# Performance work log

Hardware: AMD Instinct MI355X
Metric: run time of the kernel (lower is better)

## Reference

```python
import jax, jax.numpy as jnp
import numpy as np

N_NODES = 50000


def _add_self_loops(edge_index, num_nodes):
    loop = jnp.arange(num_nodes, dtype=edge_index.dtype)
    row = jnp.concatenate([edge_index[0], loop])
    col = jnp.concatenate([edge_index[1], loop])
    return row, col


def _gcn_norm(row, col, num_nodes):
    # deg computed on target index with unit edge weights (PyG gcn_norm)
    deg = jax.ops.segment_sum(jnp.ones_like(col, dtype=jnp.float32), col,
                              num_segments=num_nodes)
    dis = jnp.where(deg > 0, jax.lax.rsqrt(jnp.maximum(deg, 1.0)), 0.0)
    return dis[row] * dis[col]  # [E]


def _gcn_conv(x, W, b, row, col, norm, num_nodes):
    h = x @ W                                  # dense transform first (PyG order)
    msg = h[row] * norm[:, None]               # gather + normalize
    out = jax.ops.segment_sum(msg, col, num_segments=num_nodes)  # scatter-add
    return out + b


def setup_inputs() -> dict:
    key = jax.random.key(0)
    ks = jax.random.split(key, 10)
    E = 800000
    x = jax.random.normal(ks[0], (N_NODES, 29), dtype=jnp.float32)
    edge_index = jax.random.randint(ks[1], (2, E), 0, N_NODES, dtype=jnp.int64)

    def glorot(k, fan_in, fan_out):
        s = jnp.sqrt(2.0 / (fan_in + fan_out)).astype(jnp.float32)
        return jax.random.normal(k, (fan_in, fan_out), dtype=jnp.float32) * s

    return {
        "x": x, "edge_index": edge_index,
        "W1": glorot(ks[2], 29, 96),  "b1": jnp.zeros((96,), jnp.float32),
        "W2": glorot(ks[3], 96, 128), "b2": jnp.zeros((128,), jnp.float32),
        "W3": glorot(ks[4], 128, 64), "b3": jnp.zeros((64,), jnp.float32),
        "W4": glorot(ks[5], 64, 32),  "b4": jnp.zeros((32,), jnp.float32),
    }


def reference(x, edge_index, W1, b1, W2, b2, W3, b3, W4, b4):
    row, col = _add_self_loops(edge_index, N_NODES)
    norm = _gcn_norm(row, col, N_NODES)  # same graph -> same norm for all layers
    h = _gcn_conv(x, W1, b1, row, col, norm, N_NODES)
    h = jax.nn.relu(h)
    # dropout(p=0.4) is identity in eval mode
    h = _gcn_conv(h, W2, b2, row, col, norm, N_NODES)
    h = _gcn_conv(h, W3, b3, row, col, norm, N_NODES)
    h = _gcn_conv(h, W4, b4, row, col, norm, N_NODES)
    return h
```

## Files before the change

### kernel.cpp

```cpp
#include <hip/hip_runtime.h>


constexpr int NN  = 50000;
constexpr int CAP = 64;
constexpr int AGB = (NN * 8 + 255) / 256;
constexpr int C1B = (NN + 255) / 256;
constexpr int PREPB = (NN * 32 + 64 + 255) / 256;
constexpr int W34XB = 17;
constexpr int W234XB = 13;
constexpr int PGB = 128;
constexpr int SLICE = (800000 + PGB - 1) / PGB;

typedef unsigned short u16;

__global__ void place_x_kernel(const int* __restrict__ row, const int* __restrict__ col,
                               int* __restrict__ cnt, u16* __restrict__ ell, int E) {
    const int g  = blockIdx.x & 7;
    const int bi = blockIdx.x >> 3;
    const int e0 = bi * SLICE;
    int e1 = e0 + SLICE; if (e1 > E) e1 = E;
    for (int e = e0 + threadIdx.x; e < e1; e += 256) {
        const int c = col[e];
        if ((unsigned)c >= (unsigned)NN || ((c >> 6) & 7) != g) continue;
        const int r = row[e];
        if ((unsigned)r >= (unsigned)NN) continue;
        const int pos = atomicAdd(&cnt[c], 1);
        if (pos < CAP) ell[c * CAP + pos] = (u16)r;
    }
}

__global__ void prep_all_kernel(const int* __restrict__ cnt, u16* __restrict__ ell,
                                const float* __restrict__ x, float* __restrict__ dis,
                                float* __restrict__ Ba, float* __restrict__ Bb,
                                float* __restrict__ c1d,
                                const float* __restrict__ W3, const float* __restrict__ W4,
                                const float* __restrict__ b3,
                                float* __restrict__ W34, float* __restrict__ v1) {
    if (blockIdx.x >= PREPB) {
        const int wid = (blockIdx.x - PREPB) * 256 + threadIdx.x;
        if (wid < 4096) {
            const int r = wid >> 5, j = wid & 31;
            float a = 0.f;
#pragma unroll 8
            for (int k = 0; k < 64; ++k) a = fmaf(W3[r * 64 + k], W4[k * 32 + j], a);
            W34[wid] = a;
        } else if (wid < 4128) {
            const int j = wid - 4096;
            float a = 0.f;
#pragma unroll 8
            for (int k = 0; k < 64; ++k) a = fmaf(b3[k], W4[k * 32 + j], a);
            v1[j] = a;
        }
        return;
    }
    const int idx = blockIdx.x * blockDim.x + threadIdx.x;
    if (idx < NN * 32) {
        const int n = idx >> 5, f = idx & 31;
        int m = cnt[n]; if (m > CAP) m = CAP;
        const float d = rsqrtf((float)m + 1.0f);
        Ba[idx] = (f < 29) ? x[n * 29 + f] * d : 0.f;
        if (f == 31) dis[n] = d;
        if (f == 30) {
            int mp = (m + 7) & ~7; if (mp > CAP) mp = CAP;
            for (int k = m; k < mp; ++k) ell[n * CAP + k] = (u16)NN;
        }
    } else {
        const int i = idx - NN * 32;
        if (i < 32) { Ba[NN * 32 + i] = 0.f; Bb[NN * 32 + i] = 0.f; }
        else if (i == 32) dis[NN] = 0.f;
        else if (i == 33) c1d[NN] = 0.f;
    }
}

template<int MODE>
__device__ __forceinline__ void agg32_body(const float* __restrict__ hs,
                                           const int* __restrict__ cnt,
                                           const u16* __restrict__ ell,
                                           const float* __restrict__ dis,
                                           const float* __restrict__ c1,
                                           const float* __restrict__ c2,
                                           const float* __restrict__ v1,
                                           const float* __restrict__ v2,
                                           const float* __restrict__ bv,
                                           float* __restrict__ out) {
    const int idx = blockIdx.x * blockDim.x + threadIdx.x;
    if (idx >= NN * 8) return;
    const int n = idx >> 3, c = idx & 7;
    const float4* hpc = (const float4*)hs + c;
    float4 acc = hpc[n * 8];
    int m = cnt[n]; if (m > CAP) m = CAP;
    const int m8 = (m + 7) >> 3;
    const int4* ip = (const int4*)(ell + (size_t)n * CAP);
    int t = 0;
    for (; t + 2 <= m8; t += 2) {
        const int4 sA = ip[t], sB = ip[t + 1];
        const unsigned ax = (unsigned)sA.x, ay = (unsigned)sA.y;
        const unsigned az = (unsigned)sA.z, aw = (unsigned)sA.w;
        const unsigned bx = (unsigned)sB.x, by = (unsigned)sB.y;
        const unsigned bz = (unsigned)sB.z, bw = (unsigned)sB.w;
        const float4 g0 = hpc[(ax & 0xFFFFu) * 8], g1 = hpc[(ax >> 16) * 8];
        const float4 g2 = hpc[(ay & 0xFFFFu) * 8], g3 = hpc[(ay >> 16) * 8];
        const float4 g4 = hpc[(az & 0xFFFFu) * 8], g5 = hpc[(az >> 16) * 8];
        const float4 g6 = hpc[(aw & 0xFFFFu) * 8], g7 = hpc[(aw >> 16) * 8];
        const float4 h0 = hpc[(bx & 0xFFFFu) * 8], h1 = hpc[(bx >> 16) * 8];
        const float4 h2 = hpc[(by & 0xFFFFu) * 8], h3 = hpc[(by >> 16) * 8];
        const float4 h4 = hpc[(bz & 0xFFFFu) * 8], h5 = hpc[(bz >> 16) * 8];
        const float4 h6 = hpc[(bw & 0xFFFFu) * 8], h7 = hpc[(bw >> 16) * 8];
        acc.x += (((g0.x + g1.x) + (g2.x + g3.x)) + ((g4.x + g5.x) + (g6.x + g7.x)))
               + (((h0.x + h1.x) + (h2.x + h3.x)) + ((h4.x + h5.x) + (h6.x + h7.x)));
        acc.y += (((g0.y + g1.y) + (g2.y + g3.y)) + ((g4.y + g5.y) + (g6.y + g7.y)))
               + (((h0.y + h1.y) + (h2.y + h3.y)) + ((h4.y + h5.y) + (h6.y + h7.y)));
        acc.z += (((g0.z + g1.z) + (g2.z + g3.z)) + ((g4.z + g5.z) + (g6.z + g7.z)))
               + (((h0.z + h1.z) + (h2.z + h3.z)) + ((h4.z + h5.z) + (h6.z + h7.z)));
        acc.w += (((g0.w + g1.w) + (g2.w + g3.w)) + ((g4.w + g5.w) + (g6.w + g7.w)))
               + (((h0.w + h1.w) + (h2.w + h3.w)) + ((h4.w + h5.w) + (h6.w + h7.w)));
    }
    if (t < m8) {
        const int4 s = ip[t];
        const unsigned ux = (unsigned)s.x, uy = (unsigned)s.y;
        const unsigned uz = (unsigned)s.z, uw = (unsigned)s.w;
        const float4 g0 = hpc[(ux & 0xFFFFu) * 8], g1 = hpc[(ux >> 16) * 8];
        const float4 g2 = hpc[(uy & 0xFFFFu) * 8], g3 = hpc[(uy >> 16) * 8];
        const float4 g4 = hpc[(uz & 0xFFFFu) * 8], g5 = hpc[(uz >> 16) * 8];
        const float4 g6 = hpc[(uw & 0xFFFFu) * 8], g7 = hpc[(uw >> 16) * 8];
        acc.x += ((g0.x + g1.x) + (g2.x + g3.x)) + ((g4.x + g5.x) + (g6.x + g7.x));
        acc.y += ((g0.y + g1.y) + (g2.y + g3.y)) + ((g4.y + g5.y) + (g6.y + g7.y));
        acc.z += ((g0.z + g1.z) + (g2.z + g3.z)) + ((g4.z + g5.z) + (g6.z + g7.z));
        acc.w += ((g0.w + g1.w) + (g2.w + g3.w)) + ((g4.w + g5.w) + (g6.w + g7.w));
    }
    const float d = dis[n];
    float4 r;
    if (MODE == 0) {
        r.x = acc.x * d; r.y = acc.y * d; r.z = acc.z * d; r.w = acc.w * d;
    } else if (MODE == 1) {
        const float d2 = d * d;
        r.x = acc.x * d2; r.y = acc.y * d2; r.z = acc.z * d2; r.w = acc.w * d2;
    } else {
        const float a1 = c1[n], a2 = c2[n];
        const float4 w1 = ((const float4*)v1)[c];
        const float4 w2 = ((const float4*)v2)[c];
        const float4 bb = ((const float4*)bv)[c];
        r.x = fmaf(acc.x, d, fmaf(a1, w1.x, fmaf(a2, w2.x, bb.x)));
        r.y = fmaf(acc.y, d, fmaf(a1, w1.y, fmaf(a2, w2.y, bb.y)));
        r.z = fmaf(acc.z, d, fmaf(a1, w1.z, fmaf(a2, w2.z, bb.z)));
        r.w = fmaf(acc.w, d, fmaf(a1, w1.w, fmaf(a2, w2.w, bb.w)));
    }
    ((float4*)out)[idx] = r;
}

__device__ __forceinline__ void agg1_body(const float* __restrict__ in,
                                          const int* __restrict__ cnt,
                                          const u16* __restrict__ ell,
                                          const float* __restrict__ dis,
                                          float* __restrict__ out,
                                          float* __restrict__ outd, int blk0) {
    const int n = (blockIdx.x - blk0) * 256 + threadIdx.x;
    if (n >= NN) return;
    float acc = in[n];
    int m = cnt[n]; if (m > CAP) m = CAP;
    const int m8 = (m + 7) >> 3;
    const int4* ip = (const int4*)(ell + (size_t)n * CAP);
    for (int t = 0; t < m8; ++t) {
        const int4 s = ip[t];
        const unsigned ux = (unsigned)s.x, uy = (unsigned)s.y;
        const unsigned uz = (unsigned)s.z, uw = (unsigned)s.w;
        acc += ((in[ux & 0xFFFFu] + in[ux >> 16]) + (in[uy & 0xFFFFu] + in[uy >> 16]))
             + ((in[uz & 0xFFFFu] + in[uz >> 16]) + (in[uw & 0xFFFFu] + in[uw >> 16]));
    }
    const float r = dis[n] * acc;
    out[n] = r;
    if (outd) outd[n] = r * dis[n];
}

__global__ void agg_pre_kernel(const float* __restrict__ Ba, const int* __restrict__ cnt,
                               const u16* __restrict__ ell, const float* __restrict__ dis,
                               float* __restrict__ Bb, float* __restrict__ c1,
                               float* __restrict__ c1d,
                               const float* __restrict__ W2, const float* __restrict__ b2,
                               const float* __restrict__ W34, float* __restrict__ W234,
                               float* __restrict__ v2) {
    if (blockIdx.x < AGB) {
        agg32_body<0>(Ba, cnt, ell, dis, nullptr, nullptr, nullptr, nullptr, nullptr, Bb);
    } else if (blockIdx.x < AGB + C1B) {
        agg1_body(dis, cnt, ell, dis, c1, c1d, AGB);
    } else {
        const int wid = (blockIdx.x - AGB - C1B) * 256 + threadIdx.x;
        if (wid < 3072) {
            const int r = wid >> 5, j = wid & 31;
            float a = 0.f;
#pragma unroll 8
            for (int k = 0; k < 128; ++k) a = fmaf(W2[r * 128 + k], W34[k * 32 + j], a);
            W234[wid] = a;
        } else if (wid < 3104) {
            const int j = wid - 3072;
            float a = 0.f;
#pragma unroll 8
            for (int k = 0; k < 128; ++k) a = fmaf(b2[k], W34[k * 32 + j], a);
            v2[j] = a;
        }
    }
}

__global__ void agg_hop1_kernel(const float* __restrict__ Ba, const int* __restrict__ cnt,
                                const u16* __restrict__ ell, const float* __restrict__ dis,
                                float* __restrict__ Bb, const float* __restrict__ c1d,
                                float* __restrict__ c2) {
    if (blockIdx.x < AGB)
        agg32_body<1>(Ba, cnt, ell, dis, nullptr, nullptr, nullptr, nullptr, nullptr, Bb);
    else
        agg1_body(c1d, cnt, ell, dis, c2, nullptr, AGB);
}

__global__ void agg_hop2_kernel(const float* __restrict__ Bb, const int* __restrict__ cnt,
                                const u16* __restrict__ ell, const float* __restrict__ dis,
                                float* __restrict__ Ba) {
    agg32_body<1>(Bb, cnt, ell, dis, nullptr, nullptr, nullptr, nullptr, nullptr, Ba);
}

__global__ void agg_hop3_kernel(const float* __restrict__ Ba, const int* __restrict__ cnt,
                                const u16* __restrict__ ell, const float* __restrict__ dis,
                                const float* __restrict__ c1, const float* __restrict__ c2,
                                const float* __restrict__ v1, const float* __restrict__ v2,
                                const float* __restrict__ bv, float* __restrict__ out) {
    agg32_body<2>(Ba, cnt, ell, dis, c1, c2, v1, v2, bv, out);
}

__global__ void __launch_bounds__(192, 2)
gemm_fused_kernel(const float* __restrict__ X, const float* __restrict__ W1,
                  const float* __restrict__ b1, const float* __restrict__ dis,
                  const float* __restrict__ W234, float* __restrict__ G) {
    constexpr int NPB = 16, RSX = 36, RSH = 104;
    __shared__ float xs[NPB * RSX];
    __shared__ float hsm[NPB * RSH];
    const int tid = threadIdx.x;
    const int n0  = blockIdx.x * NPB;

    const float4* Xv = (const float4*)(X + (size_t)n0 * 32);
    for (int i = tid; i < NPB * 8; i += 192) {
        const int nl = i >> 3, r = i & 7;
        float4 v = make_float4(0.f, 0.f, 0.f, 0.f);
        if (n0 + nl < NN) v = Xv[nl * 8 + r];
        *(float4*)(xs + nl * RSX + r * 4) = v;
    }
    __syncthreads();

    {
        const int cg = tid % 24, g = tid / 24;
        const float* x0 = xs + (2 * g) * RSX;
        const float* x1 = x0 + RSX;
        const float4* Wv = (const float4*)W1;
        float4 a0 = make_float4(0.f, 0.f, 0.f, 0.f);
        float4 a1 = make_float4(0.f, 0.f, 0.f, 0.f);
#pragma unroll
        for (int k = 0; k < 29; ++k) {
            const float4 w = Wv[k * 24 + cg];
            const float v0 = x0[k], v1 = x1[k];
            a0.x = fmaf(v0, w.x, a0.x); a0.y = fmaf(v0, w.y, a0.y);
            a0.z = fmaf(v0, w.z, a0.z); a0.w = fmaf(v0, w.w, a0.w);
            a1.x = fmaf(v1, w.x, a1.x); a1.y = fmaf(v1, w.y, a1.y);
            a1.z = fmaf(v1, w.z, a1.z); a1.w = fmaf(v1, w.w, a1.w);
        }
        const float4 bb = ((const float4*)b1)[cg];
#pragma unroll
        for (int h = 0; h < 2; ++h) {
            const int nl = 2 * g + h, node = n0 + nl;
            const float d = (node < NN) ? dis[node] : 0.f;
            const float4 a = h ? a1 : a0;
            float4 r;
            r.x = fmaxf(a.x + bb.x, 0.f) * d; r.y = fmaxf(a.y + bb.y, 0.f) * d;
            r.z = fmaxf(a.z + bb.z, 0.f) * d; r.w = fmaxf(a.w + bb.w, 0.f) * d;
            *(float4*)(hsm + nl * RSH + cg * 4) = r;
        }
    }
    __syncthreads();

    if (tid < 128) {
        const int nl = tid >> 3, cg = tid & 7;
        const float* hr = hsm + nl * RSH;
        const float4* Wv = (const float4*)W234;
        float4 a = make_float4(0.f, 0.f, 0.f, 0.f);
#pragma unroll 8
        for (int k = 0; k < 96; ++k) {
            const float4 w = Wv[k * 8 + cg];
            const float v = hr[k];
            a.x = fmaf(v, w.x, a.x); a.y = fmaf(v, w.y, a.y);
            a.z = fmaf(v, w.z, a.z); a.w = fmaf(v, w.w, a.w);
        }
        const int node = n0 + nl;
        if (node < NN) ((float4*)(G + (size_t)node * 32))[cg] = a;
    }
}

extern "C" void kernel_launch(void* const* d_in, const int* in_sizes, int n_in,
                              void* d_out, int out_size, void* d_ws, size_t ws_size,
                              hipStream_t stream) {
    const float* x  = (const float*)d_in[0];
    const int*   ei = (const int*)d_in[1];
    const float* W1 = (const float*)d_in[2]; const float* b1 = (const float*)d_in[3];
    const float* W2 = (const float*)d_in[4]; const float* b2 = (const float*)d_in[5];
    const float* W3 = (const float*)d_in[6]; const float* b3 = (const float*)d_in[7];
    const float* W4 = (const float*)d_in[8]; const float* b4p = (const float*)d_in[9];
    float* outp = (float*)d_out;

    const int E = in_sizes[1] / 2;
    const int* row = ei;
    const int* col = ei + E;

    int*   cnt  = (int*)d_ws;
    float* dis  = (float*)(cnt + 50048);
    u16*   ell  = (u16*)(dis + 50056);
    float* c1   = (float*)((int*)ell + 1600000);
    float* c1d  = c1 + 50056;
    float* c2   = c1d + 50056;
    float* W34  = c2 + 50056;
    float* W234 = W34 + 4096;
    float* v1   = W234 + 3072;
    float* v2   = v1 + 32;
    float* Ba   = v2 + 32;
    float* Bb   = Ba + 1600064;

    hipMemsetAsync(cnt, 0, 50048 * sizeof(int), stream);
    place_x_kernel<<<8 * PGB, 256, 0, stream>>>(row, col, cnt, ell, E);
    prep_all_kernel<<<PREPB + W34XB, 256, 0, stream>>>(cnt, ell, x, dis, Ba, Bb, c1d,
                                                       W3, W4, b3, W34, v1);
    agg_pre_kernel<<<AGB + C1B + W234XB, 256, 0, stream>>>(Ba, cnt, ell, dis, Bb, c1, c1d,
                                                           W2, b2, W34, W234, v2);
    gemm_fused_kernel<<<(NN + 15) / 16, 192, 0, stream>>>(Bb, W1, b1, dis, W234, Ba);
    agg_hop1_kernel<<<AGB + C1B, 256, 0, stream>>>(Ba, cnt, ell, dis, Bb, c1d, c2);
    agg_hop2_kernel<<<AGB, 256, 0, stream>>>(Bb, cnt, ell, dis, Ba);
    agg_hop3_kernel<<<AGB, 256, 0, stream>>>(Ba, cnt, ell, dis, c1, c2, v1, v2, b4p, outp);
}
```

Measured before the change: 224.1 us.

## Split aggregation into XCD-aware half-feature blocks and vectorize edge placement

The 32-wide aggregation now maps each block to 64 nodes times half the feature chunks. The block index is arranged so that blocks on the same XCD (blockIdx mod 8) share a node range and feature half, which is meant to improve per-XCD L2 locality for neighbor gathers. ELL index loads and output stores become nontemporal to keep gather data resident in cache. Edge placement reads col/row as int4 vectors, uses twice as many blocks, and handles a scalar tail. The XCD-to-block mapping is an assumption about hardware scheduling, and nontemporal hints may not help.

```diff
diff --git a/kernel.cpp b/kernel.cpp
--- a/kernel.cpp
+++ b/kernel.cpp
@@ -3,30 +3,57 @@
 
 constexpr int NN  = 50000;
 constexpr int CAP = 64;
-constexpr int AGB = (NN * 8 + 255) / 256;
+constexpr int SUBS = (NN + 63) / 64;
+constexpr int AGB  = 8 * ((SUBS + 3) / 4);
 constexpr int C1B = (NN + 255) / 256;
 constexpr int PREPB = (NN * 32 + 64 + 255) / 256;
 constexpr int W34XB = 17;
 constexpr int W234XB = 13;
-constexpr int PGB = 128;
-constexpr int SLICE = (800000 + PGB - 1) / PGB;
+constexpr int PXB = 256;
 
 typedef unsigned short u16;
+typedef int   iv4 __attribute__((ext_vector_type(4)));
+typedef float fv4 __attribute__((ext_vector_type(4)));
 
 __global__ void place_x_kernel(const int* __restrict__ row, const int* __restrict__ col,
                                int* __restrict__ cnt, u16* __restrict__ ell, int E) {
     const int g  = blockIdx.x & 7;
     const int bi = blockIdx.x >> 3;
-    const int e0 = bi * SLICE;
-    int e1 = e0 + SLICE; if (e1 > E) e1 = E;
-    for (int e = e0 + threadIdx.x; e < e1; e += 256) {
-        const int c = col[e];
-        if ((unsigned)c >= (unsigned)NN || ((c >> 6) & 7) != g) continue;
-        const int r = row[e];
-        if ((unsigned)r >= (unsigned)NN) continue;
-        const int pos = atomicAdd(&cnt[c], 1);
-        if (pos < CAP) ell[c * CAP + pos] = (u16)r;
-    }
+    const int n4 = E >> 2;
+    const int slice = (n4 + PXB - 1) / PXB;
+    const int i0 = bi * slice;
+    int i1 = i0 + slice; if (i1 > n4) i1 = n4;
+    const iv4* cv = (const iv4*)col;
+    const iv4* rv = (const iv4*)row;
+#define PLACE1(cc, rr) {                                                        \
+        const int c_ = (cc);                                                    \
+        if ((((c_ >> 6) & 7) == g) && (unsigned)c_ < (unsigned)NN) {            \
+            const int r_ = (rr);                                               \
+            if ((unsigned)r_ < (unsigned)NN) {                                  \
+                const int pos = atomicAdd(&cnt[c_], 1);                         \
+                if (pos < CAP) ell[c_ * CAP + pos] = (u16)r_;                   \
+            }                                                                   \
+        }                                                                       \
+    }
+    for (int i = i0 + threadIdx.x; i < i1; i += 256) {
+        const iv4 c4 = cv[i];
+        const iv4 r4 = rv[i];
+        PLACE1(c4.x, r4.x);
+        PLACE1(c4.y, r4.y);
+        PLACE1(c4.z, r4.z);
+        PLACE1(c4.w, r4.w);
+    }
+    if (bi == 0) {
+        for (int e = (n4 << 2) + threadIdx.x; e < E; e += 256) {
+            const int c = col[e];
+            if (((c >> 6) & 7) != g || (unsigned)c >= (unsigned)NN) continue;
+            const int r = row[e];
+            if ((unsigned)r >= (unsigned)NN) continue;
+            const int pos = atomicAdd(&cnt[c], 1);
+            if (pos < CAP) ell[c * CAP + pos] = (u16)r;
+        }
+    }
+#undef PLACE1
 }
 
 __global__ void prep_all_kernel(const int* __restrict__ cnt, u16* __restrict__ ell,
@@ -73,7 +100,7 @@
 }
 
 template<int MODE>
-__device__ __forceinline__ void agg32_body(const float* __restrict__ hs,
+__device__ __forceinline__ void agg16_body(const float* __restrict__ hs,
                                            const int* __restrict__ cnt,
                                            const u16* __restrict__ ell,
                                            const float* __restrict__ dis,
@@ -83,17 +110,21 @@
                                            const float* __restrict__ v2,
                                            const float* __restrict__ bv,
                                            float* __restrict__ out) {
-    const int idx = blockIdx.x * blockDim.x + threadIdx.x;
-    if (idx >= NN * 8) return;
-    const int n = idx >> 3, c = idx & 7;
+    const int b   = blockIdx.x;
+    const int xcd = b & 7;
+    const int sub = (b >> 3) * 4 + (xcd & 3);
+    const int n   = sub * 64 + (threadIdx.x >> 2);
+    if (n >= NN) return;
+    const int c   = ((xcd >> 2) << 2) | (threadIdx.x & 3);
     const float4* hpc = (const float4*)hs + c;
     float4 acc = hpc[n * 8];
     int m = cnt[n]; if (m > CAP) m = CAP;
     const int m8 = (m + 7) >> 3;
-    const int4* ip = (const int4*)(ell + (size_t)n * CAP);
+    const iv4* ip = (const iv4*)(ell + (size_t)n * CAP);
     int t = 0;
     for (; t + 2 <= m8; t += 2) {
-        const int4 sA = ip[t], sB = ip[t + 1];
+        const iv4 sA = __builtin_nontemporal_load(ip + t);
+        const iv4 sB = __builtin_nontemporal_load(ip + t + 1);
         const unsigned ax = (unsigned)sA.x, ay = (unsigned)sA.y;
         const unsigned az = (unsigned)sA.z, aw = (unsigned)sA.w;
         const unsigned bx = (unsigned)sB.x, by = (unsigned)sB.y;
@@ -116,7 +147,7 @@
                + (((h0.w + h1.w) + (h2.w + h3.w)) + ((h4.w + h5.w) + (h6.w + h7.w)));
     }
     if (t < m8) {
-        const int4 s = ip[t];
+        const iv4 s = __builtin_nontemporal_load(ip + t);
         const unsigned ux = (unsigned)s.x, uy = (unsigned)s.y;
         const unsigned uz = (unsigned)s.z, uw = (unsigned)s.w;
         const float4 g0 = hpc[(ux & 0xFFFFu) * 8], g1 = hpc[(ux >> 16) * 8];
@@ -129,7 +160,7 @@
         acc.w += ((g0.w + g1.w) + (g2.w + g3.w)) + ((g4.w + g5.w) + (g6.w + g7.w));
     }
     const float d = dis[n];
-    float4 r;
+    fv4 r;
     if (MODE == 0) {
         r.x = acc.x * d; r.y = acc.y * d; r.z = acc.z * d; r.w = acc.w * d;
     } else if (MODE == 1) {
@@ -145,7 +176,7 @@
         r.z = fmaf(acc.z, d, fmaf(a1, w1.z, fmaf(a2, w2.z, bb.z)));
         r.w = fmaf(acc.w, d, fmaf(a1, w1.w, fmaf(a2, w2.w, bb.w)));
     }
-    ((float4*)out)[idx] = r;
+    __builtin_nontemporal_store(r, (fv4*)out + (size_t)n * 8 + c);
 }
 
 __device__ __forceinline__ void agg1_body(const float* __restrict__ in,
@@ -159,9 +190,9 @@
     float acc = in[n];
     int m = cnt[n]; if (m > CAP) m = CAP;
     const int m8 = (m + 7) >> 3;
-    const int4* ip = (const int4*)(ell + (size_t)n * CAP);
+    const iv4* ip = (const iv4*)(ell + (size_t)n * CAP);
     for (int t = 0; t < m8; ++t) {
-        const int4 s = ip[t];
+        const iv4 s = ip[t];
         const unsigned ux = (unsigned)s.x, uy = (unsigned)s.y;
         const unsigned uz = (unsigned)s.z, uw = (unsigned)s.w;
         acc += ((in[ux & 0xFFFFu] + in[ux >> 16]) + (in[uy & 0xFFFFu] + in[uy >> 16]))
@@ -180,7 +211,7 @@
                                const float* __restrict__ W34, float* __restrict__ W234,
                                float* __restrict__ v2) {
     if (blockIdx.x < AGB) {
-        agg32_body<0>(Ba, cnt, ell, dis, nullptr, nullptr, nullptr, nullptr, nullptr, Bb);
+        agg16_body<0>(Ba, cnt, ell, dis, nullptr, nullptr, nullptr, nullptr, nullptr, Bb);
     } else if (blockIdx.x < AGB + C1B) {
         agg1_body(dis, cnt, ell, dis, c1, c1d, AGB);
     } else {
@@ -206,7 +237,7 @@
                                 float* __restrict__ Bb, const float* __restrict__ c1d,
                                 float* __restrict__ c2) {
     if (blockIdx.x < AGB)
-        agg32_body<1>(Ba, cnt, ell, dis, nullptr, nullptr, nullptr, nullptr, nullptr, Bb);
+        agg16_body<1>(Ba, cnt, ell, dis, nullptr, nullptr, nullptr, nullptr, nullptr, Bb);
     else
         agg1_body(c1d, cnt, ell, dis, c2, nullptr, AGB);
 }
@@ -214,7 +245,7 @@
 __global__ void agg_hop2_kernel(const float* __restrict__ Bb, const int* __restrict__ cnt,
                                 const u16* __restrict__ ell, const float* __restrict__ dis,
                                 float* __restrict__ Ba) {
-    agg32_body<1>(Bb, cnt, ell, dis, nullptr, nullptr, nullptr, nullptr, nullptr, Ba);
+    agg16_body<1>(Bb, cnt, ell, dis, nullptr, nullptr, nullptr, nullptr, nullptr, Ba);
 }
 
 __global__ void agg_hop3_kernel(const float* __restrict__ Ba, const int* __restrict__ cnt,
@@ -222,7 +253,7 @@
                                 const float* __restrict__ c1, const float* __restrict__ c2,
                                 const float* __restrict__ v1, const float* __restrict__ v2,
                                 const float* __restrict__ bv, float* __restrict__ out) {
-    agg32_body<2>(Ba, cnt, ell, dis, c1, c2, v1, v2, bv, out);
+    agg16_body<2>(Ba, cnt, ell, dis, c1, c2, v1, v2, bv, out);
 }
 
 __global__ void __launch_bounds__(192, 2)
@@ -320,7 +351,7 @@
     float* Bb   = Ba + 1600064;
 
     hipMemsetAsync(cnt, 0, 50048 * sizeof(int), stream);
-    place_x_kernel<<<8 * PGB, 256, 0, stream>>>(row, col, cnt, ell, E);
+    place_x_kernel<<<8 * PXB, 256, 0, stream>>>(row, col, cnt, ell, E);
     prep_all_kernel<<<PREPB + W34XB, 256, 0, stream>>>(cnt, ell, x, dis, Ba, Bb, c1d,
                                                        W3, W4, b3, W34, v1);
     agg_pre_kernel<<<AGB + C1B + W234XB, 256, 0, stream>>>(Ba, cnt, ell, dis, Bb, c1, c1d,
```

New measurement: 260.6 us. 1.16x slower.
